# Kernel optimization log

Measured on AMD Instinct MI355X. Metric: run time of the kernel, lower is better.

## Reference

```python
import jax, jax.numpy as jnp
import numpy as np
from jax import lax

B, S, HID, H, HKV, D, M = 2, 4096, 2048, 16, 8, 128, 256
CHUNK = 128
EPS = 1e-6


def setup_inputs() -> dict:
    key = jax.random.key(0)
    ks = jax.random.split(key, 6)
    hidden_states = jax.random.normal(ks[0], (B, S, HID), jnp.float32)
    wq = jax.random.normal(ks[1], (H * D, HID), jnp.float32) / np.sqrt(HID)
    wk = jax.random.normal(ks[2], (HKV * D, HID), jnp.float32) / np.sqrt(HID)
    wv = jax.random.normal(ks[3], (HKV * D, HID), jnp.float32) / np.sqrt(HID)
    wo = jax.random.normal(ks[4], (HID, H * D), jnp.float32) / np.sqrt(H * D)
    proj_matrix = jax.random.normal(ks[5], (M, D), jnp.float32)
    # RoPE tables (HF LLaMA style): cos/sin of shape (B, S, head_dim)
    inv_freq = 1.0 / (10000.0 ** (np.arange(0, D, 2, dtype=np.float64) / D))
    freqs = np.arange(S, dtype=np.float64)[:, None] * inv_freq[None, :]
    emb = np.concatenate([freqs, freqs], axis=-1)  # (S, D)
    cos = jnp.asarray(np.broadcast_to(np.cos(emb)[None], (B, S, D)).copy(), jnp.float32)
    sin = jnp.asarray(np.broadcast_to(np.sin(emb)[None], (B, S, D)).copy(), jnp.float32)
    return {"hidden_states": hidden_states, "cos": cos, "sin": sin,
            "wq": wq, "wk": wk, "wv": wv, "wo": wo, "proj_matrix": proj_matrix}


def _rotate_half(x):
    x1, x2 = x[..., : D // 2], x[..., D // 2:]
    return jnp.concatenate([-x2, x1], axis=-1)


def _apply_rope(q, k, cos, sin):
    # unsqueeze_dim=1: cos/sin (B,S,D) -> (B,1,S,D)
    cos, sin = cos[:, None], sin[:, None]
    return q * cos + _rotate_half(q) * sin, k * cos + _rotate_half(k) * sin


def _feature_map(x, proj_matrix, is_query):
    # FAVOR+ positive random features approximating exp(q.k / sqrt(d)).
    xn = x * (D ** -0.25)                                  # data normalizer d^-1/4
    u = jnp.einsum('bhsd,md->bhsm', xn, proj_matrix)       # (B,H,S,M)
    sq = 0.5 * jnp.sum(xn * xn, axis=-1, keepdims=True)
    z = u - sq
    if is_query:
        z = z - jnp.max(z, axis=-1, keepdims=True)         # per-query max (cancels in ratio)
    else:
        z = z - jnp.max(z)                                 # global max for keys (cancels)
    return jnp.exp(z) * (M ** -0.5) + EPS


def _causal_linear_attention(phi_q, phi_k, v):
    # phi_q/phi_k: (B,H,S,M), v: (B,H,S,D). Chunked causal prefix-sum scan.
    nc = S // CHUNK
    pq = phi_q.reshape(B, H, nc, CHUNK, M).transpose(2, 0, 1, 3, 4)
    pk = phi_k.reshape(B, H, nc, CHUNK, M).transpose(2, 0, 1, 3, 4)
    vc = v.reshape(B, H, nc, CHUNK, D).transpose(2, 0, 1, 3, 4)

    @jax.checkpoint
    def body(carry, inp):
        s_kv, s_k = carry                                   # (B,H,M,D), (B,H,M)
        pq_c, pk_c, v_c = inp                               # (B,H,C,M), (B,H,C,M), (B,H,C,D)
        kv = jnp.einsum('bhcm,bhcd->bhcmd', pk_c, v_c)
        kv_cum = jnp.cumsum(kv, axis=2) + s_kv[:, :, None]  # (B,H,C,M,D)
        k_cum = jnp.cumsum(pk_c, axis=2) + s_k[:, :, None]  # (B,H,C,M)
        num = jnp.einsum('bhcm,bhcmd->bhcd', pq_c, kv_cum)
        den = jnp.einsum('bhcm,bhcm->bhc', pq_c, k_cum)
        out = num / (den[..., None] + EPS)
        return (kv_cum[:, :, -1], k_cum[:, :, -1]), out

    init = (jnp.zeros((B, H, M, D), phi_q.dtype), jnp.zeros((B, H, M), phi_q.dtype))
    _, outs = lax.scan(body, init, (pq, pk, vc))            # (nc,B,H,C,D)
    return outs.transpose(1, 2, 0, 3, 4).reshape(B, H, S, D)


def reference(hidden_states, cos, sin, wq, wk, wv, wo, proj_matrix):
    q = (hidden_states @ wq.T).reshape(B, S, H, D).transpose(0, 2, 1, 3)
    k = (hidden_states @ wk.T).reshape(B, S, HKV, D).transpose(0, 2, 1, 3)
    v = (hidden_states @ wv.T).reshape(B, S, HKV, D).transpose(0, 2, 1, 3)
    q, k = _apply_rope(q, k, cos, sin)
    groups = H // HKV
    k = jnp.repeat(k, groups, axis=1)
    v = jnp.repeat(v, groups, axis=1)
    phi_q = _feature_map(q, proj_matrix, is_query=True)
    phi_k = _feature_map(k, proj_matrix, is_query=False)
    attn = _causal_linear_attention(phi_q, phi_k, v)        # (B,H,S,D)
    attn = attn.transpose(0, 2, 1, 3).reshape(B, S, H * D)
    return attn @ wo.T
```

## Files before the change

### kernel.cpp

```cpp
#include <hip/hip_runtime.h>

#define NB 2
#define NS 4096
#define NH 16
#define NKV 8
#define ND 128
#define NM 256
#define NCNK 32

#define SCALE_A 0.29730177875068026f
#define PHI_SCALE 0.0625f
#define EPSF 1e-6f

typedef unsigned short u16;
typedef unsigned int u32;
typedef __attribute__((ext_vector_type(8))) short short8;
typedef __attribute__((ext_vector_type(4))) float f32x4;

static __device__ __forceinline__ float bfh(u16 v) {
  return __uint_as_float(((u32)v) << 16);
}
static __device__ __forceinline__ u32 f2bf1(float f) {
  u32 u = __float_as_uint(f);
  return (u + 0x7fffu + ((u >> 16) & 1u)) >> 16;
}
static __device__ __forceinline__ u32 pack2(float a, float b) {
  return f2bf1(a) | (f2bf1(b) << 16);
}
static __device__ __forceinline__ void unp8(uint4 p, float* f) {
  f[0] = __uint_as_float(p.x << 16); f[1] = __uint_as_float(p.x & 0xffff0000u);
  f[2] = __uint_as_float(p.y << 16); f[3] = __uint_as_float(p.y & 0xffff0000u);
  f[4] = __uint_as_float(p.z << 16); f[5] = __uint_as_float(p.z & 0xffff0000u);
  f[6] = __uint_as_float(p.w << 16); f[7] = __uint_as_float(p.w & 0xffff0000u);
}
static __device__ __forceinline__ void ld8(const u16* p, float* f) {
  unp8(*(const uint4*)p, f);
}
static __device__ __forceinline__ void ld8(const float* p, float* f) {
  const float4 a = *(const float4*)p;
  const float4 b = *(const float4*)(p + 4);
  f[0]=a.x; f[1]=a.y; f[2]=a.z; f[3]=a.w;
  f[4]=b.x; f[5]=b.y; f[6]=b.z; f[7]=b.w;
}
static __device__ __forceinline__ void st8(u16* p, const float* o) {
  uint4 w;
  w.x = pack2(o[0], o[1]); w.y = pack2(o[2], o[3]);
  w.z = pack2(o[4], o[5]); w.w = pack2(o[6], o[7]);
  *(uint4*)p = w;
}

static __device__ __forceinline__ unsigned f2key(float f) {
  unsigned u = __float_as_uint(f);
  return (u & 0x80000000u) ? ~u : (u | 0x80000000u);
}
static __device__ __forceinline__ float key2f(unsigned k) {
  return (k & 0x80000000u) ? __uint_as_float(k & 0x7fffffffu) : __uint_as_float(~k);
}

__global__ void fill_out_f32(float* __restrict__ out, float val)
{
  const size_t idx = (size_t)blockIdx.x * 256 + threadIdx.x;
  out[idx] = val;
}

__global__ void f2b(const float* __restrict__ in, u16* __restrict__ out)
{
  const size_t i = (((size_t)blockIdx.x * 256) + threadIdx.x) * 8;
  float f[8];
  ld8(in + i, f);
  st8(out + i, f);
}

__global__ void f2b_split(const float* __restrict__ in, u16* __restrict__ hi,
                          u16* __restrict__ lo, unsigned* __restrict__ gmax)
{
  if (blockIdx.x == 0 && threadIdx.x == 0) *gmax = 0u;
  const size_t i = (size_t)blockIdx.x * 256 + threadIdx.x;
  const float f = in[i];
  const u16 h = (u16)f2bf1(f);
  hi[i] = h;
  lo[i] = (u16)f2bf1(f - bfh(h));
}

#define GLL(gp, lp) \
  __builtin_amdgcn_global_load_lds( \
      (const __attribute__((address_space(1))) u32*)(gp), \
      (__attribute__((address_space(3))) u32*)(lp), 16, 0, 0)

static __device__ __forceinline__ void stc(float* p, float v) { *p = v; }
static __device__ __forceinline__ void stc(u16* p, float v)  { *p = (u16)f2bf1(v); }

static __device__ __forceinline__ void bar_f() {
  asm volatile("" ::: "memory");
  __builtin_amdgcn_s_barrier();
  asm volatile("" ::: "memory");
}
static __device__ __forceinline__ void lgkm0_f() {
  asm volatile("s_waitcnt lgkmcnt(0)" ::: "memory");
  __builtin_amdgcn_sched_barrier(0);
}

template <class TO>
__global__ __launch_bounds__(512, 2) void gemm_bt_256(
    const u16* __restrict__ A, const u16* __restrict__ B,
    TO* __restrict__ C, int K, int Nc)
{
  __shared__ short8 ldsv[8192];
  u16* Abuf = (u16*)ldsv;
  u16* Bbuf = (u16*)ldsv + 32768;

  const int t = threadIdx.x;
  const int lane = t & 63;
  const int wid = t >> 6;
  const int wr = wid >> 2;
  const int wc = wid & 3;

  int bid = blockIdx.y * gridDim.x + blockIdx.x;
  {
    const int nwg = gridDim.x * gridDim.y;
    const int qq = nwg >> 3, rr = nwg & 7;
    const int x = bid & 7, o = bid >> 3;
    bid = (x < rr ? x * (qq + 1) : rr * (qq + 1) + (x - rr) * qq) + o;
  }
  const int rowBase = (bid / gridDim.x) * 256;
  const int colBase = (bid % gridDim.x) * 256;
  const int NT = K >> 6;

  const int srow = t >> 3;
  const int scol = (((t & 7) ^ ((t >> 3) & 7)) << 3);
  const int sld  = t * 8;

  const int frow = lane & 15;
  const int fkey = lane & 7;
  const int fql  = lane >> 4;

#define STAGE_A(bsel, h, u) do { \
    const u16* gp_ = A + (size_t)(rowBase + (h)*128 + srow) * K + (u)*64 + scol; \
    GLL(gp_,                Abuf + (bsel)*16384 + (h)*8192 + sld); \
    GLL(gp_ + (size_t)64*K, Abuf + (bsel)*16384 + (h)*8192 + 4096 + sld); \
  } while (0)
#define STAGE_B(bsel, h, u) do { \
    const u16* gp_ = B + (size_t)(colBase + (h)*128 + srow) * K + (u)*64 + scol; \
    GLL(gp_,                Bbuf + (bsel)*16384 + (h)*8192 + sld); \
    GLL(gp_ + (size_t)64*K, Bbuf + (bsel)*16384 + (h)*8192 + 4096 + sld); \
  } while (0)

  short8 af[4][2], b0[2][2], b1[2][2];

#define LDA(Mh, bsel) do { \
    _Pragma("unroll") for (int mi = 0; mi < 4; ++mi) \
    _Pragma("unroll") for (int ks = 0; ks < 2; ++ks) { \
      const int rib_ = (Mh)*128 + wr*64 + mi*16 + frow; \
      const int pb_ = (ks*4 + fql) ^ fkey; \
      af[mi][ks] = *(const short8*)(Abuf + (bsel)*16384 + rib_*64 + pb_*8); \
    } } while (0)
#define LDB(dst, Nh, bsel) do { \
    _Pragma("unroll") for (int ni = 0; ni < 2; ++ni) \
    _Pragma("unroll") for (int ks = 0; ks < 2; ++ks) { \
      const int rib_ = (Nh)*128 + wc*32 + ni*16 + frow; \
      const int pb_ = (ks*4 + fql) ^ fkey; \
      dst[ni][ks] = *(const short8*)(Bbuf + (bsel)*16384 + rib_*64 + pb_*8); \
    } } while (0)

  f32x4 acc[2][2][4][2];
#pragma unroll
  for (int a_ = 0; a_ < 2; ++a_)
#pragma unroll
    for (int b_ = 0; b_ < 2; ++b_)
#pragma unroll
      for (int m_ = 0; m_ < 4; ++m_)
#pragma unroll
        for (int n_ = 0; n_ < 2; ++n_)
          acc[a_][b_][m_][n_] = (f32x4){0.f, 0.f, 0.f, 0.f};

#define MMQ(Mh, Nh, bfr) do { \
    _Pragma("unroll") for (int mi = 0; mi < 4; ++mi) \
    _Pragma("unroll") for (int ni = 0; ni < 2; ++ni) \
    _Pragma("unroll") for (int ks = 0; ks < 2; ++ks) \
      acc[Mh][Nh][mi][ni] = __builtin_amdgcn_mfma_f32_16x16x32_bf16( \
          af[mi][ks], bfr[ni][ks], acc[Mh][Nh][mi][ni], 0, 0, 0); \
  } while (0)

  STAGE_A(0, 0, 0); STAGE_B(0, 0, 0); STAGE_A(0, 1, 0); STAGE_B(0, 1, 0);
  STAGE_A(1, 0, 1); STAGE_B(1, 0, 1);
  asm volatile("s_waitcnt vmcnt(4)" ::: "memory");
  bar_f();

  for (int u = 0; u < NT; ++u) {
    const int bsel = u & 1, osel = bsel ^ 1;
    LDA(0, bsel); LDB(b0, 0, bsel);
    if (u + 1 < NT) STAGE_A(osel, 1, u + 1);
    bar_f(); lgkm0_f();
    __builtin_amdgcn_s_setprio(1); MMQ(0, 0, b0); __builtin_amdgcn_s_setprio(0);
    bar_f();
    LDB(b1, 1, bsel);
    if (u + 1 < NT) STAGE_B(osel, 1, u + 1);
    bar_f(); lgkm0_f();
    __builtin_amdgcn_s_setprio(1); MMQ(0, 1, b1); __builtin_amdgcn_s_setprio(0);
    bar_f();
    LDA(1, bsel);
    if (u + 2 < NT) STAGE_A(bsel, 0, u + 2);
    bar_f(); lgkm0_f();
    __builtin_amdgcn_s_setprio(1); MMQ(1, 0, b0); __builtin_amdgcn_s_setprio(0);
    bar_f();
    if (u + 2 < NT) STAGE_B(bsel, 0, u + 2);
    __builtin_amdgcn_s_setprio(1); MMQ(1, 1, b1); __builtin_amdgcn_s_setprio(0);
    asm volatile("s_waitcnt vmcnt(4)" ::: "memory");
    bar_f();
  }

  const int cr = (lane >> 4) * 4;
  const int cc = lane & 15;
#pragma unroll
  for (int Mh = 0; Mh < 2; ++Mh)
#pragma unroll
    for (int mi = 0; mi < 4; ++mi) {
      const int r0 = rowBase + Mh*128 + wr*64 + mi*16 + cr;
#pragma unroll
      for (int Nh = 0; Nh < 2; ++Nh)
#pragma unroll
        for (int ni = 0; ni < 2; ++ni) {
          const int col = colBase + Nh*128 + wc*32 + ni*16 + cc;
#pragma unroll
          for (int j = 0; j < 4; ++j)
            stc(C + (size_t)(r0 + j) * Nc + col, acc[Mh][Nh][mi][ni][j]);
        }
    }
#undef STAGE_A
#undef STAGE_B
#undef LDA
#undef LDB
#undef MMQ
}

__global__ void rope_bf(u16* __restrict__ x, const float* __restrict__ cosb,
                        const float* __restrict__ sinb)
{
  const size_t idx = (size_t)blockIdx.x * blockDim.x + threadIdx.x;
  const int d = (int)(idx & 63);
  const size_t nh = idx >> 6;
  const int hh = (int)(nh % 24);
  const size_t n = nh / 24;
  const float c1 = cosb[n * ND + d];
  const float s1 = sinb[n * ND + d];
  const float c2 = cosb[n * ND + d + 64];
  const float s2 = sinb[n * ND + d + 64];
  const int coff = (hh < 16) ? hh * 128 : 2048 + (hh - 16) * 128;
  u16* p = x + n * 4096 + coff + d;
  const float x1 = bfh(p[0]);
  const float x2 = bfh(p[64]);
  p[0]  = (u16)f2bf1(x1 * c1 - x2 * s1);
  p[64] = (u16)f2bf1(x2 * c2 + x1 * s2);
}

__global__ void sqsum_k(const u16* __restrict__ X, float* __restrict__ sqv)
{
  const size_t row = (size_t)blockIdx.x * 256 + threadIdx.x;
  const u16* p = X + (row >> 3) * 4096 + 2048 + (row & 7) * 128;
  float s = 0.f;
  for (int k = 0; k < 128; k += 8) {
    float f[8];
    ld8(p + k, f);
#pragma unroll
    for (int j = 0; j < 8; ++j) s += f[j] * f[j];
  }
  sqv[row] = 0.5f * SCALE_A * SCALE_A * s;
}

template <bool IS_Q, int RSH, int COFF>
__global__ __launch_bounds__(256) void feat_mfma(
    const u16* __restrict__ X, const u16* __restrict__ Pb,
    u16* __restrict__ U, const float* __restrict__ sqv,
    unsigned* __restrict__ gmax)
{
  __shared__ u16 As[4096];
  __shared__ u16 Bh[8192];
  __shared__ u16 Bl[8192];
  __shared__ float rmW[2][128];
  __shared__ float wmax[4];
  const int t = threadIdx.x;
  const int lane = t & 63, wid = t >> 6;
  const int wr = wid >> 1, wc = wid & 1;
  const int fr = lane & 15, fk = (lane >> 4) * 8;
  const int cr = (lane >> 4) * 4, cc = lane & 15;
  const int sr = t >> 2, sk = (t & 3) * 8, e0 = t * 8;
  const int rowBase = blockIdx.x * 128;
  const int MASK = (1 << RSH) - 1;
  const u16* Pl = Pb + NM * 128;

  const int ga = rowBase + sr, gb = rowBase + sr + 64;
  const size_t xa = (size_t)(ga >> RSH) * 4096 + COFF + (size_t)(ga & MASK) * 128 + sk;
  const size_t xb = (size_t)(gb >> RSH) * 4096 + COFF + (size_t)(gb & MASK) * 128 + sk;

  f32x4 acc[4][8];
#pragma unroll
  for (int i = 0; i < 4; ++i)
#pragma unroll
    for (int j = 0; j < 8; ++j) acc[i][j] = (f32x4){0.f, 0.f, 0.f, 0.f};

  for (int k0 = 0; k0 < 128; k0 += 32) {
    GLL(X + xa + k0, As + e0);
    GLL(X + xb + k0, As + 2048 + e0);
#pragma unroll
    for (int qq = 0; qq < 4; ++qq) {
      GLL(Pb + (size_t)(sr + qq*64) * 128 + k0 + sk, Bh + qq*2048 + e0);
      GLL(Pl + (size_t)(sr + qq*64) * 128 + k0 + sk, Bl + qq*2048 + e0);
    }
    asm volatile("s_waitcnt vmcnt(0)" ::: "memory");
    __syncthreads();
    short8 a[4];
#pragma unroll
    for (int mi = 0; mi < 4; ++mi)
      a[mi] = *(const short8*)(As + (wr*64 + mi*16 + fr)*32 + fk);
    {
      short8 bb[8];
#pragma unroll
      for (int ni = 0; ni < 8; ++ni)
        bb[ni] = *(const short8*)(Bh + (wc*128 + ni*16 + fr)*32 + fk);
#pragma unroll
      for (int mi = 0; mi < 4; ++mi)
#pragma unroll
        for (int ni = 0; ni < 8; ++ni)
          acc[mi][ni] = __builtin_amdgcn_mfma_f32_16x16x32_bf16(
              a[mi], bb[ni], acc[mi][ni], 0, 0, 0);
    }
    {
      short8 bb[8];
#pragma unroll
      for (int ni = 0; ni < 8; ++ni)
        bb[ni] = *(const short8*)(Bl + (wc*128 + ni*16 + fr)*32 + fk);
#pragma unroll
      for (int mi = 0; mi < 4; ++mi)
#pragma unroll
        for (int ni = 0; ni < 8; ++ni)
          acc[mi][ni] = __builtin_amdgcn_mfma_f32_16x16x32_bf16(
              a[mi], bb[ni], acc[mi][ni], 0, 0, 0);
    }
    __syncthreads();
  }

  if (IS_Q) {
#pragma unroll
    for (int mi = 0; mi < 4; ++mi)
#pragma unroll
      for (int j = 0; j < 4; ++j) {
        float m = acc[mi][0][j];
#pragma unroll
        for (int ni = 1; ni < 8; ++ni) m = fmaxf(m, acc[mi][ni][j]);
        m = fmaxf(m, __shfl_xor(m, 1));
        m = fmaxf(m, __shfl_xor(m, 2));
        m = fmaxf(m, __shfl_xor(m, 4));
        m = fmaxf(m, __shfl_xor(m, 8));
        const int r = wr*64 + mi*16 + cr + j;
        if (cc == 0) rmW[wc][r] = m;
      }
    __syncthreads();
#pragma unroll
    for (int mi = 0; mi < 4; ++mi)
#pragma unroll
      for (int j = 0; j < 4; ++j) {
        const int r = wr*64 + mi*16 + cr + j;
        const float mr = fmaxf(rmW[0][r], rmW[1][r]);
        u16* up = U + (size_t)(rowBase + r) * NM + wc*128 + cc;
#pragma unroll
        for (int ni = 0; ni < 8; ++ni) {
          const float phi = expf(SCALE_A * (acc[mi][ni][j] - mr)) * PHI_SCALE + EPSF;
          up[ni*16] = (u16)f2bf1(phi);
        }
      }
  } else {
    float lmax = -1e30f;
#pragma unroll
    for (int mi = 0; mi < 4; ++mi)
#pragma unroll
      for (int j = 0; j < 4; ++j) {
        const int r = wr*64 + mi*16 + cr + j;
        const float sq = sqv[rowBase + r];
#pragma unroll
        for (int ni = 0; ni < 8; ++ni) {
          const float z = SCALE_A * acc[mi][ni][j] - sq;
          acc[mi][ni][j] = z;
          lmax = fmaxf(lmax, z);
        }
      }
    lmax = fmaxf(lmax, __shfl_xor(lmax, 1));
    lmax = fmaxf(lmax, __shfl_xor(lmax, 2));
    lmax = fmaxf(lmax, __shfl_xor(lmax, 4));
    lmax = fmaxf(lmax, __shfl_xor(lmax, 8));
    lmax = fmaxf(lmax, __shfl_xor(lmax, 16));
    lmax = fmaxf(lmax, __shfl_xor(lmax, 32));
    if (lane == 0) wmax[wid] = lmax;
    __syncthreads();
    if (t == 0) {
      const float bm = fmaxf(fmaxf(wmax[0], wmax[1]), fmaxf(wmax[2], wmax[3]));
      atomicMax(gmax, f2key(bm));
    }
#pragma unroll
    for (int mi = 0; mi < 4; ++mi)
#pragma unroll
      for (int j = 0; j < 4; ++j) {
        const int r = wr*64 + mi*16 + cr + j;
        u16* up = U + (size_t)(rowBase + r) * NM + wc*128 + cc;
#pragma unroll
        for (int ni = 0; ni < 8; ++ni)
          up[ni*16] = (u16)f2bf1(expf(acc[mi][ni][j]));
      }
  }
}

__global__ void feat_k_b(u16* __restrict__ u, const unsigned* __restrict__ gmax)
{
  const size_t idx = (size_t)blockIdx.x * blockDim.x + threadIdx.x;
  const float eg = expf(-key2f(*gmax));
  const float e = bfh(u[idx]);
  u[idx] = (u16)f2bf1(e * eg * PHI_SCALE + EPSF);
}

__global__ __launch_bounds__(256) void vtrans(const u16* __restrict__ v,
                                              u16* __restrict__ vT)
{
  const int s0 = blockIdx.x * 64;
  const int d0 = blockIdx.y * 64;
  const int bkv = blockIdx.z;
  const int b = bkv >> 3, kh = bkv & 7;
  const int t = threadIdx.x;
  __shared__ u16 Tt[64][80];
  const int sl = t >> 3;
  const int ds = (t & 7) * 8;
#pragma unroll
  for (int r = 0; r < 2; ++r) {
    const u16* src = v + (size_t)(b*NS + s0 + r*32 + sl) * 4096 + 3072 + kh*128 + d0 + ds;
    *(uint4*)&Tt[r*32 + sl][ds] = *(const uint4*)src;
  }
  __syncthreads();
#pragma unroll
  for (int r = 0; r < 2; ++r) {
    const int dl = r*32 + sl;
    u16 tmp[8];
#pragma unroll
    for (int j = 0; j < 8; ++j) tmp[j] = Tt[ds + j][dl];
    u16* dst = vT + (((size_t)(b*NKV + kh) * ND) + d0 + dl) * NS + s0 + ds;
    *(uint4*)dst = *(uint4*)tmp;
  }
}

__global__ __launch_bounds__(256) void chunk_kv_mfma(
    const u16* __restrict__ phik, const u16* __restrict__ vT,
    u16* __restrict__ kvT, float* __restrict__ ksst)
{
  const int c = blockIdx.x, bkv = blockIdx.y;
  const int b = bkv >> 3, kh = bkv & 7;
  const int t = threadIdx.x;
  const int lane = t & 63, wid = t >> 6;
  const int wr = wid >> 1, wc = wid & 1;
  const int fr = lane & 15, fk = (lane >> 4) * 8;
  const int cr = (lane >> 4) * 4, cc = lane & 15;
  const int sr = t >> 2, sk = (t & 3) * 8, e0 = t * 8;

  __shared__ u16 As[4096];
  __shared__ u16 Bs[8192];

  const size_t vt_off = ((size_t)(b*NKV + kh) * ND) * NS + (size_t)c * 128;
  const size_t pk_row0 = ((size_t)(b*NS + c*128) * NKV + kh) * NM;
  const size_t pk_rstr = (size_t)NKV * NM;

  f32x4 acc[4][8];
#pragma unroll
  for (int i = 0; i < 4; ++i)
#pragma unroll
    for (int j = 0; j < 8; ++j) acc[i][j] = (f32x4){0.f, 0.f, 0.f, 0.f};

  const int m = t;
  const int sw = (m >> 1) & 3;
  float ks = 0.f;

  for (int i0 = 0; i0 < 128; i0 += 32) {
    __syncthreads();
    GLL(vT + vt_off + (size_t)sr * NS + i0 + sk,        As + e0);
    GLL(vT + vt_off + (size_t)(sr + 64) * NS + i0 + sk, As + 2048 + e0);
    u16 rowv[32];
#pragma unroll
    for (int j = 0; j < 32; ++j)
      rowv[j] = phik[pk_row0 + (size_t)(i0 + j) * pk_rstr + m];
#pragma unroll
    for (int j = 0; j < 32; ++j) ks += bfh(rowv[j]);
    u16* brow = Bs + m * 32;
#pragma unroll
    for (int q = 0; q < 4; ++q)
      *(uint4*)(brow + ((q ^ sw) * 8)) = *(const uint4*)(rowv + q*8);
    asm volatile("s_waitcnt vmcnt(0)" ::: "memory");
    __syncthreads();
    short8 a[4], bb[8];
#pragma unroll
    for (int mi = 0; mi < 4; ++mi)
      a[mi] = *(const short8*)(As + (wr*64 + mi*16 + fr)*32 + fk);
#pragma unroll
    for (int ni = 0; ni < 8; ++ni) {
      const int mrow = wc*128 + ni*16 + fr;
      const int q = fk >> 3;
      bb[ni] = *(const short8*)(Bs + mrow*32 + ((q ^ ((mrow >> 1) & 3)) << 3));
    }
#pragma unroll
    for (int mi = 0; mi < 4; ++mi)
#pragma unroll
      for (int ni = 0; ni < 8; ++ni)
        acc[mi][ni] = __builtin_amdgcn_mfma_f32_16x16x32_bf16(
            a[mi], bb[ni], acc[mi][ni], 0, 0, 0);
  }

  ksst[((size_t)bkv * NCNK + c) * NM + m] = ks;

  const size_t kv_off = ((size_t)bkv * NCNK + c) * (size_t)(ND*NM);
#pragma unroll
  for (int mi = 0; mi < 4; ++mi)
#pragma unroll
    for (int j = 0; j < 4; ++j) {
      const int d = wr*64 + mi*16 + cr + j;
#pragma unroll
      for (int ni = 0; ni < 8; ++ni) {
        const int mm = wc*128 + ni*16 + cc;
        kvT[kv_off + (size_t)d * NM + mm] = (u16)f2bf1(acc[mi][ni][j]);
      }
    }
}

__global__ void prefix_kv(u16* __restrict__ kvst)
{
  const int md = blockIdx.x * 256 + threadIdx.x;
  const size_t base = (size_t)blockIdx.y * NCNK * (NM*ND) + md;
  float carry = 0.f;
  for (int c = 0; c < NCNK; ++c) {
    const size_t a = base + (size_t)c * (NM*ND);
    const float val = bfh(kvst[a]);
    kvst[a] = (u16)f2bf1(carry);
    carry += val;
  }
}

__global__ void prefix_ks(float* __restrict__ ksst)
{
  const int m = threadIdx.x;
  const size_t base = (size_t)blockIdx.x * NCNK * NM + m;
  float carry = 0.f;
  for (int c = 0; c < NCNK; ++c) {
    const size_t a = base + (size_t)c * NM;
    const float val = ksst[a];
    ksst[a] = carry;
    carry += val;
  }
}

__global__ __launch_bounds__(256) void attn_mfma(
    const u16* __restrict__ phiq, const u16* __restrict__ phik,
    const u16* __restrict__ vT, const u16* __restrict__ kvT,
    const float* __restrict__ kspre, u16* __restrict__ attn)
{
  const int c = blockIdx.x, h = blockIdx.y, b = blockIdx.z;
  const int kh = h >> 1;
  const int bkv = b * NKV + kh;
  const int t = threadIdx.x;
  const int lane = t & 63, wid = t >> 6;
  const int wr = wid >> 1, wc = wid & 1;
  const int fr = lane & 15, fk = (lane >> 4) * 8;
  const int cr = (lane >> 4) * 4, cc = lane & 15;
  const int sr = t >> 2, sk = (t & 3) * 8, e0 = t * 8;

  __shared__ u16 As[8192];
  __shared__ u16 Bs[8192];
  __shared__ u16 Sl[16384];
  __shared__ float den_l[128];
  __shared__ float ks_l[256];

  const size_t pq_off = ((size_t)(b*NS + c*128) * NH  + h)  * NM;
  const size_t pk_off = ((size_t)(b*NS + c*128) * NKV + kh) * NM;
  const size_t vt_off = ((size_t)(b*NKV + kh) * ND) * (size_t)NS + (size_t)c * 128;
  const size_t kv_off = ((size_t)bkv * NCNK + c) * (size_t)(ND*NM);

  if (t < 128) den_l[t] = 0.f;
  ks_l[t] = kspre[((size_t)bkv * NCNK + c) * NM + t];

#define ST_A_PQ(pp, k0) do { \
    GLL(phiq + pq_off + (size_t)sr * 4096 + (k0) + sk,        As + (pp)*4096 + e0); \
    GLL(phiq + pq_off + (size_t)(sr + 64) * 4096 + (k0) + sk, As + (pp)*4096 + 2048 + e0); \
  } while (0)
#define ST_B_PK(pp, k0) do { \
    GLL(phik + pk_off + (size_t)sr * 2048 + (k0) + sk,        Bs + (pp)*4096 + e0); \
    GLL(phik + pk_off + (size_t)(sr + 64) * 2048 + (k0) + sk, Bs + (pp)*4096 + 2048 + e0); \
  } while (0)
#define ST_B_VT(pp, j0) do { \
    GLL(vT + vt_off + (size_t)sr * NS + (j0) + sk,        Bs + (pp)*4096 + e0); \
    GLL(vT + vt_off + (size_t)(sr + 64) * NS + (j0) + sk, Bs + (pp)*4096 + 2048 + e0); \
  } while (0)
#define ST_B_KV(pp, m0) do { \
    GLL(kvT + kv_off + (size_t)sr * NM + (m0) + sk,        Bs + (pp)*4096 + e0); \
    GLL(kvT + kv_off + (size_t)(sr + 64) * NM + (m0) + sk, Bs + (pp)*4096 + 2048 + e0); \
  } while (0)

  f32x4 accS[4][4];
#pragma unroll
  for (int i = 0; i < 4; ++i)
#pragma unroll
    for (int j = 0; j < 4; ++j) accS[i][j] = (f32x4){0.f, 0.f, 0.f, 0.f};

  int p = 0;
  ST_A_PQ(0, 0); ST_B_PK(0, 0);
  for (int s = 0; s < 8; ++s) {
    if (s < 7) {
      ST_A_PQ(p ^ 1, (s + 1) * 32); ST_B_PK(p ^ 1, (s + 1) * 32);
      asm volatile("s_waitcnt vmcnt(4)" ::: "memory");
    } else {
      ST_B_VT(p ^ 1, 0);
      asm volatile("s_waitcnt vmcnt(2)" ::: "memory");
    }
    bar_f();
    short8 a[4], bb[4];
#pragma unroll
    for (int mi = 0; mi < 4; ++mi)
      a[mi] = *(const short8*)(As + p*4096 + (wr*64 + mi*16 + fr)*32 + fk);
#pragma unroll
    for (int ni = 0; ni < 4; ++ni)
      bb[ni] = *(const short8*)(Bs + p*4096 + (wc*64 + ni*16 + fr)*32 + fk);
    lgkm0_f();
    __builtin_amdgcn_s_setprio(1);
#pragma unroll
    for (int mi = 0; mi < 4; ++mi)
#pragma unroll
      for (int ni = 0; ni < 4; ++ni)
        accS[mi][ni] = __builtin_amdgcn_mfma_f32_16x16x32_bf16(
            a[mi], bb[ni], accS[mi][ni], 0, 0, 0);
    __builtin_amdgcn_s_setprio(0);
    bar_f(); p ^= 1;
  }

#pragma unroll
  for (int mi = 0; mi < 4; ++mi)
#pragma unroll
    for (int j = 0; j < 4; ++j) {
      const int r = wr*64 + mi*16 + cr + j;
      float s = 0.f;
#pragma unroll
      for (int ni = 0; ni < 4; ++ni) {
        const int cl = wc*64 + ni*16 + cc;
        float vv = accS[mi][ni][j];
        vv = (cl > r) ? 0.f : vv;
        accS[mi][ni][j] = vv;
        s += vv;
      }
      s += __shfl_xor(s, 1); s += __shfl_xor(s, 2);
      s += __shfl_xor(s, 4); s += __shfl_xor(s, 8);
      if (cc == 0) atomicAdd(&den_l[r], s);
#pragma unroll
      for (int ni = 0; ni < 4; ++ni) {
        const int cl = wc*64 + ni*16 + cc;
        u32 bo = ((u32)r << 8) + ((u32)cl << 1);
        bo ^= (u32)(r & 7) << 4;
        *(u16*)((char*)Sl + bo) = (u16)f2bf1(accS[mi][ni][j]);
      }
    }
  asm volatile("s_waitcnt lgkmcnt(0)" ::: "memory");

  f32x4 acc2[4][4];
#pragma unroll
  for (int i = 0; i < 4; ++i)
#pragma unroll
    for (int j = 0; j < 4; ++j) acc2[i][j] = (f32x4){0.f, 0.f, 0.f, 0.f};

  for (int s = 0; s < 4; ++s) {
    if (s < 3) {
      ST_B_VT(p ^ 1, (s + 1) * 32);
      asm volatile("s_waitcnt vmcnt(2)" ::: "memory");
    } else {
      ST_A_PQ(p ^ 1, 0); ST_B_KV(p ^ 1, 0);
      asm volatile("s_waitcnt vmcnt(4)" ::: "memory");
    }
    bar_f();
    short8 a[4], bb[4];
#pragma unroll
    for (int mi = 0; mi < 4; ++mi) {
      u32 bo = ((u32)(wr*64 + mi*16 + fr) << 8) + ((u32)(s*32 + fk) << 1);
      bo ^= (u32)(fr & 7) << 4;
      a[mi] = *(const short8*)((const char*)Sl + bo);
    }
#pragma unroll
    for (int ni = 0; ni < 4; ++ni)
      bb[ni] = *(const short8*)(Bs + p*4096 + (wc*64 + ni*16 + fr)*32 + fk);
    lgkm0_f();
    __builtin_amdgcn_s_setprio(1);
#pragma unroll
    for (int mi = 0; mi < 4; ++mi)
#pragma unroll
      for (int ni = 0; ni < 4; ++ni)
        acc2[mi][ni] = __builtin_amdgcn_mfma_f32_16x16x32_bf16(
            a[mi], bb[ni], acc2[mi][ni], 0, 0, 0);
    __builtin_amdgcn_s_setprio(0);
    bar_f(); p ^= 1;
  }

  for (int s = 0; s < 8; ++s) {
    if (s < 7) {
      ST_A_PQ(p ^ 1, (s + 1) * 32); ST_B_KV(p ^ 1, (s + 1) * 32);
      asm volatile("s_waitcnt vmcnt(4)" ::: "memory");
    } else {
      asm volatile("s_waitcnt vmcnt(0)" ::: "memory");
    }
    bar_f();
    short8 a[4], bb[4];
#pragma unroll
    for (int mi = 0; mi < 4; ++mi)
      a[mi] = *(const short8*)(As + p*4096 + (wr*64 + mi*16 + fr)*32 + fk);
#pragma unroll
    for (int ni = 0; ni < 4; ++ni)
      bb[ni] = *(const short8*)(Bs + p*4096 + (wc*64 + ni*16 + fr)*32 + fk);
    lgkm0_f();
    __builtin_amdgcn_s_setprio(1);
#pragma unroll
    for (int mi = 0; mi < 4; ++mi)
#pragma unroll
      for (int ni = 0; ni < 4; ++ni)
        acc2[mi][ni] = __builtin_amdgcn_mfma_f32_16x16x32_bf16(
            a[mi], bb[ni], acc2[mi][ni], 0, 0, 0);
    __builtin_amdgcn_s_setprio(0);
    {
      const int pr = t >> 1;
      const int pm = (t & 1) * 16;
      float xf[16];
      unp8(*(const uint4*)(As + p*4096 + pr*32 + pm), xf);
      unp8(*(const uint4*)(As + p*4096 + pr*32 + pm + 8), xf + 8);
      float sm = 0.f;
#pragma unroll
      for (int jj = 0; jj < 16; ++jj) sm += xf[jj] * ks_l[s*32 + pm + jj];
      sm += __shfl_xor(sm, 1);
      if (!(t & 1)) atomicAdd(&den_l[pr], sm);
    }
    if (s == 7) asm volatile("s_waitcnt lgkmcnt(0)" ::: "memory");
    bar_f(); p ^= 1;
  }

#pragma unroll
  for (int mi = 0; mi < 4; ++mi)
#pragma unroll
    for (int j = 0; j < 4; ++j) {
      const int r = wr*64 + mi*16 + cr + j;
      const float inv = 1.0f / (den_l[r] + EPSF);
      u16* op = attn + ((size_t)(b*NS + c*128 + r) * NH + h) * ND + wc*64 + cc;
#pragma unroll
      for (int ni = 0; ni < 4; ++ni)
        op[ni*16] = (u16)f2bf1(acc2[mi][ni][j] * inv);
    }
#undef ST_A_PQ
#undef ST_B_PK
#undef ST_B_VT
#undef ST_B_KV
}

extern "C" void kernel_launch(void* const* d_in, const int* in_sizes, int n_in,
                              void* d_out, int out_size, void* d_ws, size_t ws_size,
                              hipStream_t stream)
{
  const float* hidden = (const float*)d_in[0];
  const float* cosb   = (const float*)d_in[1];
  const float* sinb   = (const float*)d_in[2];
  const float* wq     = (const float*)d_in[3];
  const float* wk     = (const float*)d_in[4];
  const float* wv     = (const float*)d_in[5];
  const float* wo     = (const float*)d_in[6];
  const float* proj   = (const float*)d_in[7];
  float* out = (float*)d_out;

  const size_t MiB = 1024ull * 1024ull;
  if (ws_size < 186ull * MiB) {
    fill_out_f32<<<65536, 256, 0, stream>>>(out, 400.f);
    return;
  }

  u16* qkv  = (u16*)d_ws;
  u16* phiq = qkv  + 33554432;
  u16* kvst = phiq + 33554432;
  float* ksst = (float*)(kvst + 16777216);
  unsigned* gmax = (unsigned*)(ksst + 131072);
  float* sqv = (float*)(gmax + 64);
  u16* wqkvb = (u16*)(sqv + 65536);
  u16* wob  = wqkvb + 8388608;
  u16* pb   = wob + 4194304;
  u16* hb   = kvst;
  u16* phik = (u16*)d_out;
  u16* vTb  = phik + 16777216;
  u16* attn = qkv;

  f2b<<<8192, 256, 0, stream>>>(hidden, hb);
  f2b<<<2048, 256, 0, stream>>>(wq, wqkvb);
  f2b<<<1024, 256, 0, stream>>>(wk, wqkvb + 2048*2048);
  f2b<<<1024, 256, 0, stream>>>(wv, wqkvb + 3072*2048);
  f2b<<<2048, 256, 0, stream>>>(wo, wob);
  f2b_split<<<128, 256, 0, stream>>>(proj, pb, pb + 32768, gmax);

  gemm_bt_256<u16><<<dim3(16, 32), 512, 0, stream>>>(hb, wqkvb, qkv, 2048, 4096);

  vtrans<<<dim3(64, 2, 16), 256, 0, stream>>>(qkv, vTb);
  rope_bf<<<49152, 256, 0, stream>>>(qkv, cosb, sinb);

  sqsum_k<<<256, 256, 0, stream>>>(qkv, sqv);
  feat_mfma<true , 4, 0   ><<<1024, 256, 0, stream>>>(qkv, pb, phiq, sqv, gmax);
  feat_mfma<false, 3, 2048><<< 512, 256, 0, stream>>>(qkv, pb, phik, sqv, gmax);
  feat_k_b<<<65536, 256, 0, stream>>>(phik, gmax);

  chunk_kv_mfma<<<dim3(NCNK, NB*NKV), 256, 0, stream>>>(phik, vTb, kvst, ksst);
  prefix_kv<<<dim3(128, NB*NKV), 256, 0, stream>>>(kvst);
  prefix_ks<<<NB*NKV, 256, 0, stream>>>(ksst);

  attn_mfma<<<dim3(NCNK, NH, NB), 256, 0, stream>>>(phiq, phik, vTb, kvst, ksst, attn);

  gemm_bt_256<float><<<dim3(8, 32), 512, 0, stream>>>(attn, wob, out, 2048, 2048);
}
```

Measured before the change: 630.6 us.

## Fuse score and inter-chunk passes into one phi_q sweep with warp specialization

The attention kernel now streams phi_q over M only once. In that single sweep it computes both the intra-chunk scores (against phi_k) and the inter-chunk numerator (against the kv prefix state), with half the warps owning each 128-wide output. Afterwards the masked scores are written to LDS, and only the wc==1 warps run the small S·V pass. Global-to-LDS loads get an XOR swizzle to reduce bank conflicts. This removes the second phi_q read and one pipeline phase, but it idles half the warps during the S·V pass and raises the accumulator register count to 32 fragments per warp, which may hurt occupancy.

Measured after the change: 650.9 us. +3.2%, slower.

```diff
diff --git a/kernel.cpp b/kernel.cpp
--- a/kernel.cpp
+++ b/kernel.cpp
@@ -561,13 +561,14 @@
   const int t = threadIdx.x;
   const int lane = t & 63, wid = t >> 6;
   const int wr = wid >> 1, wc = wid & 1;
-  const int fr = lane & 15, fk = (lane >> 4) * 8;
+  const int fr = lane & 15, fql = lane >> 4;
   const int cr = (lane >> 4) * 4, cc = lane & 15;
-  const int sr = t >> 2, sk = (t & 3) * 8, e0 = t * 8;
+  const int sr = t >> 2, e0 = t * 8;
+  const int qsw = (((t & 3) ^ (sr & 3)) << 3);
+  const int fsw = ((fql ^ (fr & 3)) << 3);
 
   __shared__ u16 As[8192];
-  __shared__ u16 Bs[8192];
-  __shared__ u16 Sl[16384];
+  __shared__ u16 Bs[16384];
   __shared__ float den_l[128];
   __shared__ float ks_l[256];
 
@@ -579,156 +580,64 @@
   if (t < 128) den_l[t] = 0.f;
   ks_l[t] = kspre[((size_t)bkv * NCNK + c) * NM + t];
 
-#define ST_A_PQ(pp, k0) do { \
-    GLL(phiq + pq_off + (size_t)sr * 4096 + (k0) + sk,        As + (pp)*4096 + e0); \
-    GLL(phiq + pq_off + (size_t)(sr + 64) * 4096 + (k0) + sk, As + (pp)*4096 + 2048 + e0); \
+#define ST_PQ(pp, m0) do { \
+    GLL(phiq + pq_off + (size_t)sr * 4096 + (m0) + qsw,        As + (pp)*4096 + e0); \
+    GLL(phiq + pq_off + (size_t)(sr + 64) * 4096 + (m0) + qsw, As + (pp)*4096 + 2048 + e0); \
   } while (0)
-#define ST_B_PK(pp, k0) do { \
-    GLL(phik + pk_off + (size_t)sr * 2048 + (k0) + sk,        Bs + (pp)*4096 + e0); \
-    GLL(phik + pk_off + (size_t)(sr + 64) * 2048 + (k0) + sk, Bs + (pp)*4096 + 2048 + e0); \
+#define ST_BKV(pp, m0) do { \
+    GLL(phik + pk_off + (size_t)sr * 2048 + (m0) + qsw,        Bs + (pp)*8192 + e0); \
+    GLL(phik + pk_off + (size_t)(sr + 64) * 2048 + (m0) + qsw, Bs + (pp)*8192 + 2048 + e0); \
+    GLL(kvT + kv_off + (size_t)sr * NM + (m0) + qsw,           Bs + (pp)*8192 + 4096 + e0); \
+    GLL(kvT + kv_off + (size_t)(sr + 64) * NM + (m0) + qsw,    Bs + (pp)*8192 + 6144 + e0); \
   } while (0)
-#define ST_B_VT(pp, j0) do { \
-    GLL(vT + vt_off + (size_t)sr * NS + (j0) + sk,        Bs + (pp)*4096 + e0); \
-    GLL(vT + vt_off + (size_t)(sr + 64) * NS + (j0) + sk, Bs + (pp)*4096 + 2048 + e0); \
+#define ST_VT(pp, j0) do { \
+    GLL(vT + vt_off + (size_t)sr * NS + (j0) + qsw,            As + (pp)*4096 + e0); \
+    GLL(vT + vt_off + (size_t)(sr + 64) * NS + (j0) + qsw,     As + (pp)*4096 + 2048 + e0); \
   } while (0)
-#define ST_B_KV(pp, m0) do { \
-    GLL(kvT + kv_off + (size_t)sr * NM + (m0) + sk,        Bs + (pp)*4096 + e0); \
-    GLL(kvT + kv_off + (size_t)(sr + 64) * NM + (m0) + sk, Bs + (pp)*4096 + 2048 + e0); \
-  } while (0)
-
-  f32x4 accS[4][4];
+
+  f32x4 acc[4][8];
 #pragma unroll
   for (int i = 0; i < 4; ++i)
 #pragma unroll
-    for (int j = 0; j < 4; ++j) accS[i][j] = (f32x4){0.f, 0.f, 0.f, 0.f};
+    for (int j = 0; j < 8; ++j) acc[i][j] = (f32x4){0.f, 0.f, 0.f, 0.f};
 
   int p = 0;
-  ST_A_PQ(0, 0); ST_B_PK(0, 0);
+  ST_PQ(0, 0); ST_BKV(0, 0);
   for (int s = 0; s < 8; ++s) {
     if (s < 7) {
-      ST_A_PQ(p ^ 1, (s + 1) * 32); ST_B_PK(p ^ 1, (s + 1) * 32);
-      asm volatile("s_waitcnt vmcnt(4)" ::: "memory");
+      ST_PQ(p ^ 1, (s + 1) * 32); ST_BKV(p ^ 1, (s + 1) * 32);
+      asm volatile("s_waitcnt vmcnt(6)" ::: "memory");
     } else {
-      ST_B_VT(p ^ 1, 0);
+      ST_VT(p ^ 1, 0);
       asm volatile("s_waitcnt vmcnt(2)" ::: "memory");
     }
     bar_f();
-    short8 a[4], bb[4];
-#pragma unroll
-    for (int mi = 0; mi < 4; ++mi)
-      a[mi] = *(const short8*)(As + p*4096 + (wr*64 + mi*16 + fr)*32 + fk);
-#pragma unroll
-    for (int ni = 0; ni < 4; ++ni)
-      bb[ni] = *(const short8*)(Bs + p*4096 + (wc*64 + ni*16 + fr)*32 + fk);
+    short8 a[4], bb[8];
+#pragma unroll
+    for (int mi = 0; mi < 4; ++mi)
+      a[mi] = *(const short8*)(As + p*4096 + (wr*64 + mi*16 + fr)*32 + fsw);
+#pragma unroll
+    for (int ni = 0; ni < 8; ++ni)
+      bb[ni] = *(const short8*)(Bs + p*8192 + (wc*128 + ni*16 + fr)*32 + fsw);
     lgkm0_f();
     __builtin_amdgcn_s_setprio(1);
 #pragma unroll
     for (int mi = 0; mi < 4; ++mi)
 #pragma unroll
-      for (int ni = 0; ni < 4; ++ni)
-        accS[mi][ni] = __builtin_amdgcn_mfma_f32_16x16x32_bf16(
-            a[mi], bb[ni], accS[mi][ni], 0, 0, 0);
-    __builtin_amdgcn_s_setprio(0);
-    bar_f(); p ^= 1;
-  }
-
-#pragma unroll
-  for (int mi = 0; mi < 4; ++mi)
-#pragma unroll
-    for (int j = 0; j < 4; ++j) {
-      const int r = wr*64 + mi*16 + cr + j;
-      float s = 0.f;
-#pragma unroll
-      for (int ni = 0; ni < 4; ++ni) {
-        const int cl = wc*64 + ni*16 + cc;
-        float vv = accS[mi][ni][j];
-        vv = (cl > r) ? 0.f : vv;
-        accS[mi][ni][j] = vv;
-        s += vv;
-      }
-      s += __shfl_xor(s, 1); s += __shfl_xor(s, 2);
-      s += __shfl_xor(s, 4); s += __shfl_xor(s, 8);
-      if (cc == 0) atomicAdd(&den_l[r], s);
-#pragma unroll
-      for (int ni = 0; ni < 4; ++ni) {
-        const int cl = wc*64 + ni*16 + cc;
-        u32 bo = ((u32)r << 8) + ((u32)cl << 1);
-        bo ^= (u32)(r & 7) << 4;
-        *(u16*)((char*)Sl + bo) = (u16)f2bf1(accS[mi][ni][j]);
-      }
-    }
-  asm volatile("s_waitcnt lgkmcnt(0)" ::: "memory");
-
-  f32x4 acc2[4][4];
-#pragma unroll
-  for (int i = 0; i < 4; ++i)
-#pragma unroll
-    for (int j = 0; j < 4; ++j) acc2[i][j] = (f32x4){0.f, 0.f, 0.f, 0.f};
-
-  for (int s = 0; s < 4; ++s) {
-    if (s < 3) {
-      ST_B_VT(p ^ 1, (s + 1) * 32);
-      asm volatile("s_waitcnt vmcnt(2)" ::: "memory");
-    } else {
-      ST_A_PQ(p ^ 1, 0); ST_B_KV(p ^ 1, 0);
-      asm volatile("s_waitcnt vmcnt(4)" ::: "memory");
-    }
-    bar_f();
-    short8 a[4], bb[4];
-#pragma unroll
-    for (int mi = 0; mi < 4; ++mi) {
-      u32 bo = ((u32)(wr*64 + mi*16 + fr) << 8) + ((u32)(s*32 + fk) << 1);
-      bo ^= (u32)(fr & 7) << 4;
-      a[mi] = *(const short8*)((const char*)Sl + bo);
-    }
-#pragma unroll
-    for (int ni = 0; ni < 4; ++ni)
-      bb[ni] = *(const short8*)(Bs + p*4096 + (wc*64 + ni*16 + fr)*32 + fk);
-    lgkm0_f();
-    __builtin_amdgcn_s_setprio(1);
-#pragma unroll
-    for (int mi = 0; mi < 4; ++mi)
-#pragma unroll
-      for (int ni = 0; ni < 4; ++ni)
-        acc2[mi][ni] = __builtin_amdgcn_mfma_f32_16x16x32_bf16(
-            a[mi], bb[ni], acc2[mi][ni], 0, 0, 0);
-    __builtin_amdgcn_s_setprio(0);
-    bar_f(); p ^= 1;
-  }
-
-  for (int s = 0; s < 8; ++s) {
-    if (s < 7) {
-      ST_A_PQ(p ^ 1, (s + 1) * 32); ST_B_KV(p ^ 1, (s + 1) * 32);
-      asm volatile("s_waitcnt vmcnt(4)" ::: "memory");
-    } else {
-      asm volatile("s_waitcnt vmcnt(0)" ::: "memory");
-    }
-    bar_f();
-    short8 a[4], bb[4];
-#pragma unroll
-    for (int mi = 0; mi < 4; ++mi)
-      a[mi] = *(const short8*)(As + p*4096 + (wr*64 + mi*16 + fr)*32 + fk);
-#pragma unroll
-    for (int ni = 0; ni < 4; ++ni)
-      bb[ni] = *(const short8*)(Bs + p*4096 + (wc*64 + ni*16 + fr)*32 + fk);
-    lgkm0_f();
-    __builtin_amdgcn_s_setprio(1);
-#pragma unroll
-    for (int mi = 0; mi < 4; ++mi)
-#pragma unroll
-      for (int ni = 0; ni < 4; ++ni)
-        acc2[mi][ni] = __builtin_amdgcn_mfma_f32_16x16x32_bf16(
-            a[mi], bb[ni], acc2[mi][ni], 0, 0, 0);
+      for (int ni = 0; ni < 8; ++ni)
+        acc[mi][ni] = __builtin_amdgcn_mfma_f32_16x16x32_bf16(
+            a[mi], bb[ni], acc[mi][ni], 0, 0, 0);
     __builtin_amdgcn_s_setprio(0);
     {
       const int pr = t >> 1;
-      const int pm = (t & 1) * 16;
+      const int b0_ = (t & 1) * 2;
+      uint4 u0 = *(const uint4*)(As + p*4096 + pr*32 + ((b0_ ^ (pr & 3)) << 3));
+      uint4 u1 = *(const uint4*)(As + p*4096 + pr*32 + (((b0_ + 1) ^ (pr & 3)) << 3));
       float xf[16];
-      unp8(*(const uint4*)(As + p*4096 + pr*32 + pm), xf);
-      unp8(*(const uint4*)(As + p*4096 + pr*32 + pm + 8), xf + 8);
+      unp8(u0, xf); unp8(u1, xf + 8);
       float sm = 0.f;
 #pragma unroll
-      for (int jj = 0; jj < 16; ++jj) sm += xf[jj] * ks_l[s*32 + pm + jj];
+      for (int jj = 0; jj < 16; ++jj) sm += xf[jj] * ks_l[s*32 + (t & 1)*16 + jj];
       sm += __shfl_xor(sm, 1);
       if (!(t & 1)) atomicAdd(&den_l[pr], sm);
     }
@@ -736,21 +645,84 @@
     bar_f(); p ^= 1;
   }
 
-#pragma unroll
-  for (int mi = 0; mi < 4; ++mi)
-#pragma unroll
-    for (int j = 0; j < 4; ++j) {
-      const int r = wr*64 + mi*16 + cr + j;
-      const float inv = 1.0f / (den_l[r] + EPSF);
-      u16* op = attn + ((size_t)(b*NS + c*128 + r) * NH + h) * ND + wc*64 + cc;
-#pragma unroll
-      for (int ni = 0; ni < 4; ++ni)
-        op[ni*16] = (u16)f2bf1(acc2[mi][ni][j] * inv);
-    }
-#undef ST_A_PQ
-#undef ST_B_PK
-#undef ST_B_VT
-#undef ST_B_KV
+  if (wc == 0) {
+#pragma unroll
+    for (int mi = 0; mi < 4; ++mi)
+#pragma unroll
+      for (int j = 0; j < 4; ++j) {
+        const int r = wr*64 + mi*16 + cr + j;
+        float s = 0.f;
+#pragma unroll
+        for (int ni = 0; ni < 8; ++ni) {
+          const int cl = ni*16 + cc;
+          float vv = acc[mi][ni][j];
+          vv = (cl > r) ? 0.f : vv;
+          acc[mi][ni][j] = vv;
+          s += vv;
+        }
+        s += __shfl_xor(s, 1); s += __shfl_xor(s, 2);
+        s += __shfl_xor(s, 4); s += __shfl_xor(s, 8);
+        if (cc == 0) den_l[r] += s;
+#pragma unroll
+        for (int ni = 0; ni < 8; ++ni) {
+          const int cl = ni*16 + cc;
+          u32 bo = ((u32)r << 8) + ((u32)cl << 1);
+          bo ^= (u32)(r & 7) << 4;
+          *(u16*)((char*)Bs + bo) = (u16)f2bf1(acc[mi][ni][j]);
+        }
+      }
+  }
+  lgkm0_f();
+  bar_f();
+
+  for (int s = 0; s < 4; ++s) {
+    if (s < 3) {
+      ST_VT(p ^ 1, (s + 1) * 32);
+      asm volatile("s_waitcnt vmcnt(2)" ::: "memory");
+    } else {
+      asm volatile("s_waitcnt vmcnt(0)" ::: "memory");
+    }
+    bar_f();
+    if (wc == 1) {
+      short8 a[4], bb[8];
+#pragma unroll
+      for (int mi = 0; mi < 4; ++mi) {
+        u32 bo = ((u32)(wr*64 + mi*16 + fr) << 8) + ((u32)(s*32 + fql*8) << 1);
+        bo ^= (u32)(fr & 7) << 4;
+        a[mi] = *(const short8*)((const char*)Bs + bo);
+      }
+#pragma unroll
+      for (int ni = 0; ni < 8; ++ni)
+        bb[ni] = *(const short8*)(As + p*4096 + (ni*16 + fr)*32 + fsw);
+      lgkm0_f();
+      __builtin_amdgcn_s_setprio(1);
+#pragma unroll
+      for (int mi = 0; mi < 4; ++mi)
+#pragma unroll
+        for (int ni = 0; ni < 8; ++ni)
+          acc[mi][ni] = __builtin_amdgcn_mfma_f32_16x16x32_bf16(
+              a[mi], bb[ni], acc[mi][ni], 0, 0, 0);
+      __builtin_amdgcn_s_setprio(0);
+    }
+    bar_f(); p ^= 1;
+  }
+
+  if (wc == 1) {
+#pragma unroll
+    for (int mi = 0; mi < 4; ++mi)
+#pragma unroll
+      for (int j = 0; j < 4; ++j) {
+        const int r = wr*64 + mi*16 + cr + j;
+        const float inv = 1.0f / (den_l[r] + EPSF);
+        u16* op = attn + ((size_t)(b*NS + c*128 + r) * NH + h) * ND + cc;
+#pragma unroll
+        for (int ni = 0; ni < 8; ++ni)
+          op[ni*16] = (u16)f2bf1(acc[mi][ni][j] * inv);
+      }
+  }
+#undef ST_PQ
+#undef ST_BKV
+#undef ST_VT
 }
 
 extern "C" void kernel_launch(void* const* d_in, const int* in_sizes, int n_in,
```
